# Performance work log

Measured on AMD Instinct MI355X. Metric: run time of the kernel, lower is better.

The kernel has to match this reference:

```python
import jax, jax.numpy as jnp
import numpy as np

N = 100000   # nodes
E = 1600000  # edges
F = 128      # in_feats
H = 4        # heads
D = 32       # out_feats per head
NEG_SLOPE = 0.2


def setup_inputs() -> dict:
    key = jax.random.key(0)
    k1, k2, k3, k4, k5, k6 = jax.random.split(key, 6)
    feat = jax.random.normal(k1, (N, F), dtype=jnp.float32)
    W = jax.random.normal(k2, (H * D, F), dtype=jnp.float32) * (1.0 / np.sqrt(F))
    attn_l = jax.random.normal(k3, (1, H, D), dtype=jnp.float32) * 0.1
    attn_r = jax.random.normal(k4, (1, H, D), dtype=jnp.float32) * 0.1
    src = jax.random.randint(k5, (E,), 0, N, dtype=jnp.int32)
    dst = jax.random.randint(k6, (E,), 0, N, dtype=jnp.int32)
    return {"feat": feat, "W": W, "attn_l": attn_l, "attn_r": attn_r, "src": src, "dst": dst}


def reference(feat, W, attn_l, attn_r, src, dst):
    # fc projection: [N, F] -> [N, H, D]
    h = (feat @ W.T).reshape(N, H, D)
    # per-node attention logits [N, H]
    el = jnp.sum(h * attn_l, axis=-1)
    er = jnp.sum(h * attn_r, axis=-1)
    # edge scores: el[src] + er[dst] -> leaky relu  [E, H]
    e = jax.nn.leaky_relu(el[src] + er[dst], negative_slope=NEG_SLOPE)
    # segment softmax over edges grouped by destination node, per head
    m = jax.ops.segment_max(e, dst, num_segments=N)          # [N, H]
    ex = jnp.exp(e - m[dst])                                 # [E, H]
    s = jax.ops.segment_sum(ex, dst, num_segments=N)         # [N, H]
    alpha = ex / s[dst]                                      # [E, H]
    # weighted sparse aggregation: out[dst] += alpha * h[src]
    msgs = alpha[:, :, None] * h[src]                        # [E, H, D]
    rst = jax.ops.segment_sum(msgs, dst, num_segments=N)     # [N, H, D]
    return rst
```

## Files before the change

kernel.cpp:

```cpp
#include <hip/hip_runtime.h>

constexpr int N_NODES = 100000;
constexpr int E_EDGES = 1600000;
constexpr int NBLK    = (N_NODES + 1023) / 1024;
constexpr int NBLOCKS = (N_NODES + 63) / 64;

typedef _Float16 f16;
typedef _Float16 f16x2 __attribute__((ext_vector_type(2)));
typedef _Float16 f16x4 __attribute__((ext_vector_type(4)));
typedef _Float16 f16x8 __attribute__((ext_vector_type(8)));
typedef float f32x4 __attribute__((ext_vector_type(4)));

__device__ __forceinline__ void hist_phase(int bid, int tid,
                                           const int4* __restrict__ dst4,
                                           int* __restrict__ deg,
                                           int4* __restrict__ rank4) {
    int t = bid * 256 + tid;
    if (t < E_EDGES / 4) {
        int4 d = dst4[t];
        int r0 = atomicAdd(&deg[d.x], 1);
        int r1 = atomicAdd(&deg[d.y], 1);
        int r2 = atomicAdd(&deg[d.z], 1);
        int r3 = atomicAdd(&deg[d.w], 1);
        rank4[t] = make_int4(r0, r1, r2, r3);
    }
}

__device__ __forceinline__ void gemm_phase(int bid, int tid, f16* Wlds,
                                           const float* __restrict__ feat,
                                           const float* __restrict__ W,
                                           const float* __restrict__ attn_l,
                                           const float* __restrict__ attn_r,
                                           f16* __restrict__ h2,
                                           float* __restrict__ el,
                                           float* __restrict__ er) {
    char* wb = (char*)Wlds;
    {
        int n = tid >> 1;
        int kh = (tid & 1) * 64;
        const float* wsrc = W + n * 128 + kh;
#pragma unroll
        for (int q = 0; q < 8; ++q) {
            float4 u0 = *reinterpret_cast<const float4*>(wsrc + q * 8);
            float4 u1 = *reinterpret_cast<const float4*>(wsrc + q * 8 + 4);
            f16x8 v;
            v[0] = (f16)u0.x; v[1] = (f16)u0.y; v[2] = (f16)u0.z; v[3] = (f16)u0.w;
            v[4] = (f16)u1.x; v[5] = (f16)u1.y; v[6] = (f16)u1.z; v[7] = (f16)u1.w;
            unsigned byte = (unsigned)(n * 256 + kh * 2 + q * 16) ^ ((n & 7) << 4);
            *reinterpret_cast<f16x8*>(wb + byte) = v;
        }
    }
    __syncthreads();

    const int wav  = tid >> 6;
    const int lane = tid & 63;
    const int la = lane & 15;
    const int lb = lane >> 4;
    const int row0w = bid * 64 + wav * 16;

    f16x8 ffrag[4];
    {
        int rowA = row0w + la;
        if (rowA >= N_NODES) rowA = N_NODES - 1;
        const float* ap = feat + (size_t)rowA * 128 + lb * 8;
#pragma unroll
        for (int kk = 0; kk < 4; ++kk) {
            float4 u0 = *reinterpret_cast<const float4*>(ap + kk * 32);
            float4 u1 = *reinterpret_cast<const float4*>(ap + kk * 32 + 4);
            f16x8 a;
            a[0] = (f16)u0.x; a[1] = (f16)u0.y; a[2] = (f16)u0.z; a[3] = (f16)u0.w;
            a[4] = (f16)u1.x; a[5] = (f16)u1.y; a[6] = (f16)u1.z; a[7] = (f16)u1.w;
            ffrag[kk] = a;
        }
    }

    f32x4 acc[8];
#pragma unroll
    for (int t = 0; t < 8; ++t) acc[t] = (f32x4){0.f, 0.f, 0.f, 0.f};

#pragma unroll
    for (int t = 0; t < 8; ++t) {
        int wrow = t * 16 + la;
#pragma unroll
        for (int kk = 0; kk < 4; ++kk) {
            unsigned byte = (unsigned)(wrow * 256 + (kk * 32 + lb * 8) * 2) ^ ((wrow & 7) << 4);
            f16x8 b = *reinterpret_cast<const f16x8*>(wb + byte);
            acc[t] = __builtin_amdgcn_mfma_f32_16x16x32_f16(b, ffrag[kk], acc[t], 0, 0, 0);
        }
    }

    const int row = row0w + la;
    const bool ok = row < N_NODES;
    if (ok) {
#pragma unroll
        for (int t = 0; t < 8; ++t) {
            f16x4 hv;
            hv.x = (f16)acc[t][0]; hv.y = (f16)acc[t][1];
            hv.z = (f16)acc[t][2]; hv.w = (f16)acc[t][3];
            *reinterpret_cast<f16x4*>(&h2[(size_t)row * 128 + t * 16 + lb * 4]) = hv;
        }
    }

    float sl[4] = {0.f, 0.f, 0.f, 0.f}, sr[4] = {0.f, 0.f, 0.f, 0.f};
#pragma unroll
    for (int t = 0; t < 8; ++t) {
        float4 alv = reinterpret_cast<const float4*>(attn_l)[t * 4 + lb];
        float4 arv = reinterpret_cast<const float4*>(attn_r)[t * 4 + lb];
        int g = t >> 1;
        sl[g] += acc[t][0] * alv.x + acc[t][1] * alv.y + acc[t][2] * alv.z + acc[t][3] * alv.w;
        sr[g] += acc[t][0] * arv.x + acc[t][1] * arv.y + acc[t][2] * arv.z + acc[t][3] * arv.w;
    }
#pragma unroll
    for (int g = 0; g < 4; ++g) {
        sl[g] += __shfl_xor(sl[g], 16, 64);
        sl[g] += __shfl_xor(sl[g], 32, 64);
        sr[g] += __shfl_xor(sr[g], 16, 64);
        sr[g] += __shfl_xor(sr[g], 32, 64);
    }
    if (lb == 0 && ok) {
        *reinterpret_cast<float4*>(el + (size_t)row * 4) = make_float4(sl[0], sl[1], sl[2], sl[3]);
        *reinterpret_cast<float4*>(er + (size_t)row * 4) = make_float4(sr[0], sr[1], sr[2], sr[3]);
    }
}

__global__ __launch_bounds__(256) void k_gemm_hist(
        const float* __restrict__ feat, const float* __restrict__ W,
        const float* __restrict__ attn_l, const float* __restrict__ attn_r,
        f16* __restrict__ h2, float* __restrict__ el, float* __restrict__ er,
        const int4* __restrict__ dst4, int* __restrict__ deg,
        int4* __restrict__ rank4) {
    __shared__ f16 Wlds[128 * 128];
    const int bid = blockIdx.x;
    const int tid = threadIdx.x;
    if (bid & 1) {
        hist_phase(bid, tid, dst4, deg, rank4);
        gemm_phase(bid, tid, Wlds, feat, W, attn_l, attn_r, h2, el, er);
    } else {
        gemm_phase(bid, tid, Wlds, feat, W, attn_l, attn_r, h2, el, er);
        hist_phase(bid, tid, dst4, deg, rank4);
    }
}

__global__ void k_bsum(const int* __restrict__ deg, int* __restrict__ aux) {
    int tid = threadIdx.x;
    int i0 = blockIdx.x * 1024 + tid * 4;
    int sum = 0;
#pragma unroll
    for (int j = 0; j < 4; ++j)
        if (i0 + j < N_NODES) sum += (deg[i0 + j] + 3) & ~3;
#pragma unroll
    for (int m = 32; m; m >>= 1) sum += __shfl_xor(sum, m, 64);
    __shared__ int wsums[4];
    if ((tid & 63) == 0) wsums[tid >> 6] = sum;
    __syncthreads();
    if (tid == 0) aux[blockIdx.x] = wsums[0] + wsums[1] + wsums[2] + wsums[3];
}

__global__ void k_bscan(const int* __restrict__ deg, const int* __restrict__ aux,
                        int* __restrict__ start, int* __restrict__ ssrc,
                        f16* __restrict__ h2, float* __restrict__ el) {
    if (blockIdx.x == 0 && threadIdx.x == 0) {
        float4 z = make_float4(0.f, 0.f, 0.f, 0.f);
        float4* hrow = reinterpret_cast<float4*>(h2 + (size_t)N_NODES * 128);
#pragma unroll
        for (int q = 0; q < 16; ++q) hrow[q] = z;
        *reinterpret_cast<float4*>(el + (size_t)N_NODES * 4) =
            make_float4(-1e4f, -1e4f, -1e4f, -1e4f);
    }
    int tid = threadIdx.x;
    int lane = tid & 63;
    int wid = tid >> 6;

    __shared__ int sbase;
    if (tid < 64) {
        int a = 0;
        if (tid < blockIdx.x) a += aux[tid];
        if (tid + 64 < blockIdx.x) a += aux[tid + 64];
#pragma unroll
        for (int m = 32; m; m >>= 1) a += __shfl_xor(a, m, 64);
        if (tid == 0) sbase = a;
    }

    int i0 = blockIdx.x * 1024 + tid * 4;
    int v[4], pv[4];
#pragma unroll
    for (int j = 0; j < 4; ++j) {
        v[j]  = (i0 + j < N_NODES) ? deg[i0 + j] : 0;
        pv[j] = (v[j] + 3) & ~3;
    }
    int tsum = pv[0] + pv[1] + pv[2] + pv[3];
    int x = tsum;
#pragma unroll
    for (int d = 1; d < 64; d <<= 1) {
        int t = __shfl_up(x, d, 64);
        if (lane >= d) x += t;
    }
    __shared__ int wsums[4];
    if (lane == 63) wsums[wid] = x;
    __syncthreads();
    int base = sbase;
#pragma unroll
    for (int w = 0; w < 4; ++w)
        if (w < wid) base += wsums[w];
    int p = base + x - tsum;
#pragma unroll
    for (int j = 0; j < 4; ++j) {
        if (i0 + j < N_NODES) {
            start[i0 + j] = p;
            for (int q = v[j]; q < pv[j]; ++q) ssrc[p + q] = N_NODES;
        }
        p += pv[j];
    }
}

__global__ void k_scatter(const int4* __restrict__ src4, const int4* __restrict__ dst4,
                          const int4* __restrict__ rank4, const int* __restrict__ start,
                          int* __restrict__ ssrc) {
    int t = blockIdx.x * blockDim.x + threadIdx.x;
    if (t >= E_EDGES / 4) return;
    int4 s = src4[t];
    int4 d = dst4[t];
    int4 r = rank4[t];
    int p0 = start[d.x] + r.x;
    int p1 = start[d.y] + r.y;
    int p2 = start[d.z] + r.z;
    int p3 = start[d.w] + r.w;
    ssrc[p0] = s.x;
    ssrc[p1] = s.y;
    ssrc[p2] = s.z;
    ssrc[p3] = s.w;
}

__global__ __launch_bounds__(128) void k_aggr(const f16* __restrict__ h2,
                                              const float* __restrict__ el,
                                              const float* __restrict__ er,
                                              const int* __restrict__ ssrc,
                                              const int* __restrict__ start,
                                              const int* __restrict__ deg,
                                              float* __restrict__ out) {
    int n = blockIdx.x * 2 + (threadIdx.x >> 6);
    if (n >= N_NODES) return;
    int lane = threadIdx.x & 63;
    int half = lane >> 5;
    int l5 = lane & 31;
    int g = l5 >> 3;
    int d = deg[n];
    int nit = ((d + 3) & ~3) >> 2;
    int s4 = __builtin_amdgcn_readfirstlane(start[n] >> 2);
    const int4* ssrc4 = reinterpret_cast<const int4*>(ssrc);
    float ern = er[n * 4 + g];

    f16x4 acA = {0, 0, 0, 0}, acB = {0, 0, 0, 0};
    float swA = 0.f, swB = 0.f;

    if (nit > 0) {
        int4 sv = ssrc4[s4];
        for (int it = 0; it < nit; ++it) {
            int4 svn = ssrc4[s4 + it + 1];

            int nA = half ? sv.y : sv.x;
            int nB = half ? sv.w : sv.z;
            float eA = el[(size_t)nA * 4 + g];
            float eB = el[(size_t)nB * 4 + g];
            f16x4 qA = *reinterpret_cast<const f16x4*>(h2 + (size_t)nA * 128 + l5 * 4);
            f16x4 qB = *reinterpret_cast<const f16x4*>(h2 + (size_t)nB * 128 + l5 * 4);

            float xA = eA + ern; xA = fmaxf(xA, 0.2f * xA);
            float xB = eB + ern; xB = fmaxf(xB, 0.2f * xB);
            float wA = __expf(xA);
            float wB = __expf(xB);

            f16 hA = (f16)wA; f16x4 wvA = {hA, hA, hA, hA};
            f16 hB = (f16)wB; f16x4 wvB = {hB, hB, hB, hB};
            acA += wvA * qA; swA += wA;
            acB += wvB * qB; swB += wB;

            sv = svn;
        }
    }

    f16x4 ac = acA + acB;
    float swv = swA + swB;
    union { f16x4 v; int u[2]; } uu; uu.v = ac;
    int o0 = __shfl_xor(uu.u[0], 32, 64);
    int o1 = __shfl_xor(uu.u[1], 32, 64);
    union { int u[2]; f16x4 v; } vv; vv.u[0] = o0; vv.u[1] = o1;
    ac += vv.v;
    swv += __shfl_xor(swv, 32, 64);

    float inv = (d > 0) ? 1.0f / swv : 0.0f;
    if (half == 0) {
        float4 o = make_float4((float)ac[0] * inv, (float)ac[1] * inv,
                               (float)ac[2] * inv, (float)ac[3] * inv);
        *reinterpret_cast<float4*>(out + (size_t)n * 128 + l5 * 4) = o;
    }
}

extern "C" void kernel_launch(void* const* d_in, const int* in_sizes, int n_in,
                              void* d_out, int out_size, void* d_ws, size_t ws_size,
                              hipStream_t stream) {
    const float* feat   = (const float*)d_in[0];
    const float* W      = (const float*)d_in[1];
    const float* attn_l = (const float*)d_in[2];
    const float* attn_r = (const float*)d_in[3];
    const int*   src    = (const int*)d_in[4];
    const int*   dst    = (const int*)d_in[5];
    float* out = (float*)d_out;

    f16*   h2    = (f16*)d_ws;
    float* el    = (float*)(h2 + (size_t)(N_NODES + 8) * 128);
    float* er    = el + (size_t)(N_NODES + 4) * 4;
    int*   deg   = (int*)(er + (size_t)N_NODES * 4);
    int*   start = deg + N_NODES;
    int*   rank  = start + N_NODES;
    int*   ssrc  = rank + E_EDGES;
    int*   aux   = ssrc + E_EDGES + 3 * N_NODES + 64;

    hipMemsetAsync(deg, 0, N_NODES * sizeof(int), stream);

    k_gemm_hist<<<NBLOCKS, 256, 0, stream>>>(feat, W, attn_l, attn_r, h2, el, er,
                                             (const int4*)dst, deg, (int4*)rank);
    k_bsum<<<NBLK, 256, 0, stream>>>(deg, aux);
    k_bscan<<<NBLK, 256, 0, stream>>>(deg, aux, start, ssrc, h2, el);
    k_scatter<<<(E_EDGES / 4 + 255) / 256, 256, 0, stream>>>(
        (const int4*)src, (const int4*)dst, (const int4*)rank, start, ssrc);
    k_aggr<<<(N_NODES + 1) / 2, 128, 0, stream>>>(h2, el, er, ssrc, start, deg, out);
}
```

Before: 188.4 us.

## Split fused gemm/histogram kernel into separate hist and gemm launches

Replaces the combined kernel, which ran the degree histogram and the projection GEMM side by side in alternating block orders, with two kernels. A standalone histogram kernel now gives each thread 16 edges and issues all loads before the atomics to get more memory-level parallelism, followed by a separate GEMM kernel. This removes the LDS footprint and GEMM register pressure from the atomic-heavy histogram work, but adds a launch and gives up the overlap between the compute-bound GEMM and the atomic histogram.

New measurement: 211.5 us. 1.12x slower.

```diff
diff --git a/kernel.cpp b/kernel.cpp
--- a/kernel.cpp
+++ b/kernel.cpp
@@ -3,7 +3,8 @@
 constexpr int N_NODES = 100000;
 constexpr int E_EDGES = 1600000;
 constexpr int NBLK    = (N_NODES + 1023) / 1024;
-constexpr int NBLOCKS = (N_NODES + 63) / 64;
+constexpr int E4      = E_EDGES / 4;
+constexpr int HBLK    = (E4 + 1023) / 1024;
 
 typedef _Float16 f16;
 typedef _Float16 f16x2 __attribute__((ext_vector_type(2)));
@@ -11,30 +12,17 @@
 typedef _Float16 f16x8 __attribute__((ext_vector_type(8)));
 typedef float f32x4 __attribute__((ext_vector_type(4)));
 
-__device__ __forceinline__ void hist_phase(int bid, int tid,
-                                           const int4* __restrict__ dst4,
-                                           int* __restrict__ deg,
-                                           int4* __restrict__ rank4) {
-    int t = bid * 256 + tid;
-    if (t < E_EDGES / 4) {
-        int4 d = dst4[t];
-        int r0 = atomicAdd(&deg[d.x], 1);
-        int r1 = atomicAdd(&deg[d.y], 1);
-        int r2 = atomicAdd(&deg[d.z], 1);
-        int r3 = atomicAdd(&deg[d.w], 1);
-        rank4[t] = make_int4(r0, r1, r2, r3);
-    }
-}
-
-__device__ __forceinline__ void gemm_phase(int bid, int tid, f16* Wlds,
-                                           const float* __restrict__ feat,
-                                           const float* __restrict__ W,
-                                           const float* __restrict__ attn_l,
-                                           const float* __restrict__ attn_r,
-                                           f16* __restrict__ h2,
-                                           float* __restrict__ el,
-                                           float* __restrict__ er) {
+__global__ __launch_bounds__(256) void k_gemm(const float* __restrict__ feat,
+                                              const float* __restrict__ W,
+                                              const float* __restrict__ attn_l,
+                                              const float* __restrict__ attn_r,
+                                              f16* __restrict__ h2,
+                                              float* __restrict__ el,
+                                              float* __restrict__ er) {
+    __shared__ f16 Wlds[128 * 128];
     char* wb = (char*)Wlds;
+    const int tid = threadIdx.x;
+
     {
         int n = tid >> 1;
         int kh = (tid & 1) * 64;
@@ -56,7 +44,7 @@
     const int lane = tid & 63;
     const int la = lane & 15;
     const int lb = lane >> 4;
-    const int row0w = bid * 64 + wav * 16;
+    const int row0w = blockIdx.x * 64 + wav * 16;
 
     f16x8 ffrag[4];
     {
@@ -123,22 +111,31 @@
     }
 }
 
-__global__ __launch_bounds__(256) void k_gemm_hist(
-        const float* __restrict__ feat, const float* __restrict__ W,
-        const float* __restrict__ attn_l, const float* __restrict__ attn_r,
-        f16* __restrict__ h2, float* __restrict__ el, float* __restrict__ er,
-        const int4* __restrict__ dst4, int* __restrict__ deg,
-        int4* __restrict__ rank4) {
-    __shared__ f16 Wlds[128 * 128];
-    const int bid = blockIdx.x;
-    const int tid = threadIdx.x;
-    if (bid & 1) {
-        hist_phase(bid, tid, dst4, deg, rank4);
-        gemm_phase(bid, tid, Wlds, feat, W, attn_l, attn_r, h2, el, er);
-    } else {
-        gemm_phase(bid, tid, Wlds, feat, W, attn_l, attn_r, h2, el, er);
-        hist_phase(bid, tid, dst4, deg, rank4);
-    }
+__global__ __launch_bounds__(256) void k_hist(const int4* __restrict__ dst4,
+                                              int* __restrict__ deg,
+                                              int4* __restrict__ rank4) {
+    int i0 = blockIdx.x * 1024 + threadIdx.x;
+    int4 d[4];
+    bool v[4];
+#pragma unroll
+    for (int k = 0; k < 4; ++k) {
+        int idx = i0 + k * 256;
+        v[k] = idx < E4;
+        d[k] = v[k] ? dst4[idx] : make_int4(0, 0, 0, 0);
+    }
+    int4 r[4];
+#pragma unroll
+    for (int k = 0; k < 4; ++k) {
+        if (v[k]) {
+            r[k].x = atomicAdd(&deg[d[k].x], 1);
+            r[k].y = atomicAdd(&deg[d[k].y], 1);
+            r[k].z = atomicAdd(&deg[d[k].z], 1);
+            r[k].w = atomicAdd(&deg[d[k].w], 1);
+        }
+    }
+#pragma unroll
+    for (int k = 0; k < 4; ++k)
+        if (v[k]) rank4[i0 + k * 256] = r[k];
 }
 
 __global__ void k_bsum(const int* __restrict__ deg, int* __restrict__ aux) {
@@ -217,7 +214,7 @@
                           const int4* __restrict__ rank4, const int* __restrict__ start,
                           int* __restrict__ ssrc) {
     int t = blockIdx.x * blockDim.x + threadIdx.x;
-    if (t >= E_EDGES / 4) return;
+    if (t >= E4) return;
     int4 s = src4[t];
     int4 d = dst4[t];
     int4 r = rank4[t];
@@ -318,11 +315,11 @@
 
     hipMemsetAsync(deg, 0, N_NODES * sizeof(int), stream);
 
-    k_gemm_hist<<<NBLOCKS, 256, 0, stream>>>(feat, W, attn_l, attn_r, h2, el, er,
-                                             (const int4*)dst, deg, (int4*)rank);
+    k_hist<<<HBLK, 256, 0, stream>>>((const int4*)dst, deg, (int4*)rank);
+    k_gemm<<<(N_NODES + 63) / 64, 256, 0, stream>>>(feat, W, attn_l, attn_r, h2, el, er);
     k_bsum<<<NBLK, 256, 0, stream>>>(deg, aux);
     k_bscan<<<NBLK, 256, 0, stream>>>(deg, aux, start, ssrc, h2, el);
-    k_scatter<<<(E_EDGES / 4 + 255) / 256, 256, 0, stream>>>(
+    k_scatter<<<(E4 + 255) / 256, 256, 0, stream>>>(
         (const int4*)src, (const int4*)dst, (const int4*)rank, start, ssrc);
     k_aggr<<<(N_NODES + 1) / 2, 128, 0, stream>>>(h2, el, er, ssrc, start, deg, out);
 }
```
